# Optimization experiments

Measured on AMD Instinct MI355X. Metric: run time of the kernel, lower is better.

Reference implementation:

```python
import jax, jax.numpy as jnp
import numpy as np

B, N, C, K, TOPK = 16, 4096, 256, 8, 2
EPS = 1e-6
RATIO = 0.1      # gate_geno_ratio
TEMP = 1.0       # gate_temperature


def setup_inputs() -> dict:
    key = jax.random.key(0)
    ks = jax.random.split(key, 8)
    s = np.float32(1.0 / np.sqrt(C))  # ~xavier scale for C->C linears
    return {
        "tokens": jax.random.normal(ks[0], (B, N, C), jnp.float32),
        "geno_vec": jax.random.normal(ks[1], (B, C), jnp.float32),
        # gate params (gate_proj init std=0.001; gate_geno given small random instead of exact-zero init so it contributes)
        "Wg": jax.random.normal(ks[2], (K, C), jnp.float32) * 0.001,
        "bg": jnp.zeros((K,), jnp.float32),
        "Wgg": jax.random.normal(ks[3], (K, C), jnp.float32) * 0.001,
        "bgg": jnp.zeros((K,), jnp.float32),
        # per-expert 2-layer MLP params (dropout inactive in eval)
        "W1": jax.random.normal(ks[4], (K, C, C), jnp.float32) * s,
        "b1": jnp.zeros((K, C), jnp.float32),
        "W2": jax.random.normal(ks[5], (K, C, C), jnp.float32) * s,
        "b2": jnp.zeros((K, C), jnp.float32),
    }


def reference(tokens, geno_vec, Wg, bg, Wgg, bgg, W1, b1, W2, b2):
    # gate logits: [B,N,K]
    logits = jnp.einsum("bnc,kc->bnk", tokens, Wg) + bg
    logits = logits + RATIO * (geno_vec @ Wgg.T + bgg)[:, None, :]
    logits = logits / TEMP

    topv, topi = jax.lax.top_k(logits, TOPK)          # [B,N,TOPK]
    topw = jax.nn.softmax(topv, axis=-1)
    topw = jnp.maximum(topw, EPS)
    topw = topw / topw.sum(-1, keepdims=True)

    # dense gate weight matrix W: [B,N,K] (scatter of topw at topi; topk indices are distinct)
    hot = jax.nn.one_hot(topi, K, dtype=tokens.dtype)  # [B,N,TOPK,K]
    Wmat = (hot * topw[..., None]).sum(-2)             # [B,N,K]

    # load-balance loss on hard usage (detached in original)
    usage = jax.lax.stop_gradient(hot.sum(-2).mean((0, 1)))  # [K]
    lb_loss = (jnp.std(usage) / (usage.mean() + EPS)) ** 2

    mass_sum = Wmat.sum(axis=1)                        # [B,K]

    # per-expert MLP computed densely over all tokens; zero gate weight kills
    # non-routed tokens exactly (same math as gather->MLP->scatter-add)
    def expert_center(k):
        h = jax.nn.relu(tokens @ W1[k].T + b1[k])      # [B,N,C]
        out = h @ W2[k].T + b2[k]                      # [B,N,C]
        return jnp.einsum("bn,bnc->bc", Wmat[:, :, k], out)

    centers_sum = jnp.stack([expert_center(k) for k in range(K)], axis=1)  # [B,K,C]
    centers = centers_sum / jnp.maximum(mass_sum, EPS)[..., None]

    routing_confidence = (topv[:, :, 0] - topv[:, :, 1]).mean()
    return centers, lb_loss, routing_confidence
```

## Files before the change

### kernel.cpp

```cpp
#include <hip/hip_runtime.h>

#define B_ 16
#define N_ 4096
#define C_ 256
#define K_ 8
#define EPS 1e-6f
#define RATIO 0.1f

typedef float f32x4 __attribute__((ext_vector_type(4)));
typedef __bf16 bf16x8 __attribute__((ext_vector_type(8)));

__device__ inline unsigned short f2bf(float f){
  unsigned int u = __float_as_uint(f);
  u += 0x7FFFu + ((u >> 16) & 1u);
  return (unsigned short)(u >> 16);
}
__device__ inline float bf2f(unsigned short h){
  return __uint_as_float(((unsigned int)h) << 16);
}

union BFu { ushort4 u4[2]; bf16x8 v; };

__global__ __launch_bounds__(256) void k0_prep(
    const float* __restrict__ W1, const float* __restrict__ Wg,
    const float* __restrict__ geno, const float* __restrict__ Wgg,
    const float* __restrict__ bgg,
    unsigned short* __restrict__ W1swz,
    unsigned short* __restrict__ Wgp_hi, unsigned short* __restrict__ Wgp_lo,
    int* __restrict__ cnt,
    float* __restrict__ mass, float* __restrict__ conf,
    float* __restrict__ glog)
{
  int gid = blockIdx.x * 256 + threadIdx.x;
  if (gid < B_*K_) { cnt[gid] = 0; mass[gid] = 0.f; }
  if (gid == 0) conf[0] = 0.f;
  {
    int o = gid << 3;
    int lane6 = (o >> 3) & 63;
    int s  = (o >> 9) & 7;
    int nt = (o >> 12) & 15;
    int k  = o >> 16;
    int quad = lane6 >> 4, l16 = lane6 & 15;
    int j  = nt*16 + l16;
    int c0 = s*32 + quad*8;
    const float* src = W1 + (k << 16) + (j << 8) + c0;
    unsigned short* dst = W1swz + o;
    #pragma unroll
    for (int e = 0; e < 8; ++e) dst[e] = f2bf(src[e]);
  }
  if (gid < 16*C_){
    int r = gid >> 8, c = gid & 255;
    float v = (r < K_) ? Wg[(r << 8) + c] : 0.f;
    unsigned short h = f2bf(v);
    Wgp_hi[gid] = h;
    Wgp_lo[gid] = f2bf(v - bf2f(h));
  }
  int wv = gid >> 6;
  if (wv < B_*K_){
    int lane = threadIdx.x & 63;
    int b = wv >> 3, k = wv & 7;
    float4 a = *(const float4*)(geno + b*C_ + lane*4);
    float4 w = *(const float4*)(Wgg  + k*C_ + lane*4);
    float p = a.x*w.x + a.y*w.y + a.z*w.z + a.w*w.w;
    #pragma unroll
    for (int off = 32; off; off >>= 1) p += __shfl_xor(p, off);
    if (lane == 0) glog[wv] = RATIO * (p + bgg[k]);
  }
}

__global__ __launch_bounds__(256) void k1_gate(
    const float* __restrict__ tokens,
    const unsigned short* __restrict__ Wgp_hi, const unsigned short* __restrict__ Wgp_lo,
    const float* __restrict__ bg, const float* __restrict__ glog,
    int* __restrict__ cnt, int* __restrict__ bidx, float* __restrict__ bw,
    float* __restrict__ mass, float* __restrict__ conf,
    unsigned short* __restrict__ tok_bf)
{
  __shared__ float ls[64][9];
  __shared__ float bg_s[K_], gl_s[K_], mass_s[K_];
  __shared__ int lcnt[K_], gbase[K_];
  __shared__ int e0s[64], e1s[64], s0s[64], s1s[64];
  __shared__ float w0s[64], w1s[64];
  __shared__ float cred[4];
  int tid = threadIdx.x, lane = tid & 63, wave = tid >> 6;
  int quad = lane >> 4, l16 = lane & 15;
  int b = blockIdx.x >> 6;
  int tok0 = (blockIdx.x & 63) * 64;
  if (tid < K_){ bg_s[tid] = bg[tid]; gl_s[tid] = glog[b*K_ + tid];
                 mass_s[tid] = 0.f; lcnt[tid] = 0; }
  __syncthreads();

  {
    int trow = tok0 + wave*16 + l16;
    const float* xsrc = tokens + ((size_t)b*N_ + trow)*C_ + quad*8;
    unsigned short* bdst = tok_bf + (((size_t)(b*N_ + trow)) << 8) + quad*8;
    f32x4 xa[8], xb[8];
    #pragma unroll
    for (int s = 0; s < 8; ++s){
      xa[s] = *(const f32x4*)(xsrc + s*32);
      xb[s] = *(const f32x4*)(xsrc + s*32 + 4);
    }
    asm volatile("" : "+v"(xa[0]), "+v"(xa[1]), "+v"(xa[2]), "+v"(xa[3]),
                      "+v"(xa[4]), "+v"(xa[5]), "+v"(xa[6]), "+v"(xa[7]));
    asm volatile("" : "+v"(xb[0]), "+v"(xb[1]), "+v"(xb[2]), "+v"(xb[3]),
                      "+v"(xb[4]), "+v"(xb[5]), "+v"(xb[6]), "+v"(xb[7]));
    f32x4 acc; acc.x = 0.f; acc.y = 0.f; acc.z = 0.f; acc.w = 0.f;
    #pragma unroll
    for (int s = 0; s < 8; ++s){
      BFu hi, lo;
      hi.u4[0].x = f2bf(xa[s][0]); hi.u4[0].y = f2bf(xa[s][1]);
      hi.u4[0].z = f2bf(xa[s][2]); hi.u4[0].w = f2bf(xa[s][3]);
      hi.u4[1].x = f2bf(xb[s][0]); hi.u4[1].y = f2bf(xb[s][1]);
      hi.u4[1].z = f2bf(xb[s][2]); hi.u4[1].w = f2bf(xb[s][3]);
      lo.u4[0].x = f2bf(xa[s][0] - bf2f(hi.u4[0].x));
      lo.u4[0].y = f2bf(xa[s][1] - bf2f(hi.u4[0].y));
      lo.u4[0].z = f2bf(xa[s][2] - bf2f(hi.u4[0].z));
      lo.u4[0].w = f2bf(xa[s][3] - bf2f(hi.u4[0].w));
      lo.u4[1].x = f2bf(xb[s][0] - bf2f(hi.u4[1].x));
      lo.u4[1].y = f2bf(xb[s][1] - bf2f(hi.u4[1].y));
      lo.u4[1].z = f2bf(xb[s][2] - bf2f(hi.u4[1].z));
      lo.u4[1].w = f2bf(xb[s][3] - bf2f(hi.u4[1].w));
      *(ushort4*)(bdst + s*32)     = hi.u4[0];
      *(ushort4*)(bdst + s*32 + 4) = hi.u4[1];
      bf16x8 bhi = *(const bf16x8*)(Wgp_hi + l16*C_ + s*32 + quad*8);
      bf16x8 blo = *(const bf16x8*)(Wgp_lo + l16*C_ + s*32 + quad*8);
      acc = __builtin_amdgcn_mfma_f32_16x16x32_bf16(hi.v, bhi, acc, 0, 0, 0);
      acc = __builtin_amdgcn_mfma_f32_16x16x32_bf16(lo.v, bhi, acc, 0, 0, 0);
      acc = __builtin_amdgcn_mfma_f32_16x16x32_bf16(hi.v, blo, acc, 0, 0, 0);
    }
    if (l16 < K_){
      #pragma unroll
      for (int rr = 0; rr < 4; ++rr){
        int tl = wave*16 + quad*4 + rr;
        ls[tl][l16] = acc[rr] + bg_s[l16] + gl_s[l16];
      }
    }
  }
  __syncthreads();

  if (quad == 0){
    int t = (wave << 4) | l16;
    float v0 = -1e30f, v1 = -1e30f; int i0 = 0, i1 = 0;
    #pragma unroll
    for (int kk = 0; kk < K_; ++kk){
      float l = ls[t][kk];
      if (l > v0){ v1 = v0; i1 = i0; v0 = l; i0 = kk; }
      else if (l > v1){ v1 = l; i1 = kk; }
    }
    float e  = expf(v1 - v0);
    float w0 = 1.f / (1.f + e), w1 = e / (1.f + e);
    w0 = fmaxf(w0, EPS); w1 = fmaxf(w1, EPS);
    float inv = 1.f / (w0 + w1);
    w0 *= inv; w1 *= inv;
    int p0 = atomicAdd(&lcnt[i0], 1);
    int p1 = atomicAdd(&lcnt[i1], 1);
    e0s[t] = i0; e1s[t] = i1; s0s[t] = p0; s1s[t] = p1;
    w0s[t] = w0; w1s[t] = w1;
    atomicAdd(&mass_s[i0], w0);
    atomicAdd(&mass_s[i1], w1);
    float ca = v0 - v1;
    #pragma unroll
    for (int off = 8; off; off >>= 1) ca += __shfl_down(ca, off);
    if (l16 == 0) cred[wave] = ca;
  }
  __syncthreads();
  if (tid < K_){
    gbase[tid] = atomicAdd(&cnt[b*K_ + tid], lcnt[tid]);
    atomicAdd(&mass[b*K_ + tid], mass_s[tid]);
  }
  if (tid == 0) atomicAdd(conf, cred[0] + cred[1] + cred[2] + cred[3]);
  __syncthreads();
  if (quad == 0){
    int t = (wave << 4) | l16;
    int n = tok0 + t;
    int ke0 = e0s[t], ke1 = e1s[t];
    size_t o0 = (size_t)(b*K_ + ke0)*N_ + gbase[ke0] + s0s[t];
    size_t o1 = (size_t)(b*K_ + ke1)*N_ + gbase[ke1] + s1s[t];
    bidx[o0] = n;  bw[o0] = w0s[t];
    bidx[o1] = n;  bw[o1] = w1s[t];
  }
}

#define K4_STAGE(T, REG) do {                                                  \
    _Pragma("unroll")                                                          \
    for (int i = 0; i < 2; ++i){                                               \
      int c16 = (T)*512 + i*256 + tid;                                         \
      __builtin_amdgcn_global_load_lds(                                        \
        (const __attribute__((address_space(1))) unsigned int*)(wsrc + c16*8), \
        (__attribute__((address_space(3))) unsigned int*)(&Bs[REG][0] + (i*256 + tid)*8), \
        16, 0, 0);                                                             \
    }                                                                          \
  } while(0)

__global__ __launch_bounds__(256, 4) void k4_expert(
    const unsigned short* __restrict__ tok_bf, const unsigned short* __restrict__ W1swz,
    const float* __restrict__ b1, const int* __restrict__ cnt,
    const int* __restrict__ bidx, const float* __restrict__ bw,
    float* __restrict__ gpart)
{
  __shared__ unsigned short Bs[4][4096];
  __shared__ float wtok[128];
  __shared__ float red[2][4][16];
  __shared__ int Pb[129];

  int tid = threadIdx.x, lane = tid & 63, wave = tid >> 6;
  int quad = lane >> 4, l16 = lane & 15;

  if (wave == 0){
    int b2i = lane << 1;
    int cA = (cnt[b2i] + 127) >> 7;
    int cB = (cnt[b2i + 1] + 127) >> 7;
    int s = cA + cB;
    int ps = s;
    #pragma unroll
    for (int off = 1; off < 64; off <<= 1){
      int t = __shfl_up(ps, off);
      if (lane >= off) ps += t;
    }
    Pb[b2i]     = ps - s;
    Pb[b2i + 1] = ps - cB;
    if (lane == 63) Pb[128] = ps;
  }
  __syncthreads();

  int T = Pb[128];
  int lin = blockIdx.x;
  int wq = (lin & 7) * 144 + (lin >> 3);
  if (wq >= T) return;
  int lo = 0, hi = 128;
  #pragma unroll
  for (int it = 0; it < 7; ++it){
    int mid = (lo + hi) >> 1;
    if (Pb[mid] <= wq) lo = mid; else hi = mid;
  }
  int bucket = lo;
  int chunk = wq - Pb[lo];
  int bat = bucket >> 3, k = bucket & 7;
  int M = cnt[bucket];
  int Mm1 = M - 1;
  int bwbase = bucket << 12;

  const unsigned short* wsrc = W1swz + ((size_t)k << 16);

  K4_STAGE(0, 0);
  K4_STAGE(1, 1);

  if (tid < 128){
    int tn = chunk*128 + tid;
    wtok[tid] = (tn < M) ? bw[bwbase + tn] : 0.f;
  }

  int r0 = chunk*128 + (wave << 4) + l16;
  int nn0 = bidx[bwbase + min(r0, Mm1)];
  int nn1 = bidx[bwbase + min(r0 + 64, Mm1)];
  const unsigned short* p0 = tok_bf + (((size_t)((bat << 12) + nn0)) << 8) + (quad << 3);
  const unsigned short* p1 = tok_bf + (((size_t)((bat << 12) + nn1)) << 8) + (quad << 3);
  bf16x8 a0[8], a1[8];
  #pragma unroll
  for (int s = 0; s < 8; ++s){
    a0[s] = *(const bf16x8*)(p0 + s*32);
    a1[s] = *(const bf16x8*)(p1 + s*32);
  }

  float bias[16];
  #pragma unroll
  for (int p = 0; p < 16; ++p) bias[p] = b1[(k << 8) + (p << 4) + l16];

  float* gdst = gpart + (size_t)(((bucket << 5) + chunk) << 8);
  int wq4 = (wave << 4) + (quad << 2);

  #pragma unroll
  for (int p = 0; p < 16; ++p){
    if (p < 14){
      K4_STAGE(p + 2, (p + 2) & 3);
      asm volatile("s_waitcnt vmcnt(4) lgkmcnt(0)" ::: "memory");
    } else if (p == 14){
      asm volatile("s_waitcnt vmcnt(2) lgkmcnt(0)" ::: "memory");
    } else {
      asm volatile("s_waitcnt vmcnt(0) lgkmcnt(0)" ::: "memory");
    }
    __builtin_amdgcn_s_barrier();

    if (p > 0 && tid < 16){
      int pb = (p - 1) & 1;
      float sv = red[pb][0][tid] + red[pb][1][tid]
               + red[pb][2][tid] + red[pb][3][tid];
      gdst[((p - 1) << 4) + tid] = sv;
    }

    f32x4 acc0, acc1;
    acc0.x=0.f; acc0.y=0.f; acc0.z=0.f; acc0.w=0.f;
    acc1.x=0.f; acc1.y=0.f; acc1.z=0.f; acc1.w=0.f;
    #pragma unroll
    for (int s = 0; s < 8; ++s){
      bf16x8 bb = *(const bf16x8*)(&Bs[p & 3][0] + ((s*64 + lane) << 3));
      acc0 = __builtin_amdgcn_mfma_f32_16x16x32_bf16(a0[s], bb, acc0, 0, 0, 0);
      acc1 = __builtin_amdgcn_mfma_f32_16x16x32_bf16(a1[s], bb, acc1, 0, 0, 0);
    }
    float pt = 0.f;
    #pragma unroll
    for (int rr = 0; rr < 4; ++rr){
      float h0 = fmaxf(acc0[rr] + bias[p], 0.f);
      float h1 = fmaxf(acc1[rr] + bias[p], 0.f);
      pt += wtok[wq4 + rr] * h0 + wtok[64 + wq4 + rr] * h1;
    }
    pt += __shfl_down(pt, 32);
    pt += __shfl_down(pt, 16);
    if (lane < 16) red[p & 1][wave][lane] = pt;
  }
  asm volatile("s_waitcnt lgkmcnt(0)" ::: "memory");
  __builtin_amdgcn_s_barrier();
  if (tid < 16){
    float sv = red[1][0][tid] + red[1][1][tid] + red[1][2][tid] + red[1][3][tid];
    gdst[(15 << 4) + tid] = sv;
  }
}

__global__ __launch_bounds__(256) void k5_centers(
    const float* __restrict__ gpart, const int* __restrict__ cnt,
    const float* __restrict__ W2, const float* __restrict__ b2,
    const float* __restrict__ mass, const float* __restrict__ conf,
    float* __restrict__ out)
{
  __shared__ float gv[C_];
  int z = blockIdx.x, tid = threadIdx.x;
  int k = z & 7;
  int nch = (cnt[z] + 127) >> 7;
  float sv = 0.f;
  for (int c = 0; c < nch; ++c)
    sv += gpart[(size_t)((((z << 5) + c) << 8) + tid)];
  gv[tid] = sv;
  __syncthreads();
  float m = mass[z];
  float inv = 1.f / fmaxf(m, EPS);
  int tq = tid & 3, cb = tid >> 2;
  #pragma unroll 1
  for (int h = 0; h < 2; ++h){
    int c = (blockIdx.y*2 + h)*64 + cb;
    const float4* wrow = (const float4*)(W2 + ((((k << 8) + c)) << 8));
    float dot = 0.f;
    #pragma unroll
    for (int jj = 0; jj < 16; ++jj){
      float4 w4 = wrow[jj*4 + tq];
      float4 g4 = *(const float4*)&gv[(jj*4 + tq) * 4];
      dot += w4.x*g4.x + w4.y*g4.y + w4.z*g4.z + w4.w*g4.w;
    }
    dot += __shfl_xor(dot, 1);
    dot += __shfl_xor(dot, 2);
    if (tq == 0) out[z*C_ + c] = (dot + m * b2[k*C_ + c]) * inv;
  }
  if (z == 0 && blockIdx.y == 0 && tid == 0){
    float u[K_];
    #pragma unroll
    for (int kk = 0; kk < K_; ++kk) u[kk] = 0.f;
    for (int i = 0; i < B_*K_; ++i) u[i & 7] += (float)cnt[i];
    float mean = 0.f;
    #pragma unroll
    for (int kk = 0; kk < K_; ++kk){ u[kk] *= (1.f / (float)(B_*N_)); mean += u[kk]; }
    mean *= (1.f / K_);
    float var = 0.f;
    #pragma unroll
    for (int kk = 0; kk < K_; ++kk){ float d = u[kk] - mean; var += d*d; }
    var *= (1.f / K_);
    float denom = mean + EPS;
    out[B_*K_*C_]     = var / (denom * denom);
    out[B_*K_*C_ + 1] = conf[0] / (float)(B_*N_);
  }
}

extern "C" void kernel_launch(void* const* d_in, const int* in_sizes, int n_in,
                              void* d_out, int out_size, void* d_ws, size_t ws_size,
                              hipStream_t stream)
{
  const float* tokens = (const float*)d_in[0];
  const float* geno   = (const float*)d_in[1];
  const float* Wg     = (const float*)d_in[2];
  const float* bg     = (const float*)d_in[3];
  const float* Wgg    = (const float*)d_in[4];
  const float* bgg    = (const float*)d_in[5];
  const float* W1     = (const float*)d_in[6];
  const float* b1     = (const float*)d_in[7];
  const float* W2     = (const float*)d_in[8];
  const float* b2     = (const float*)d_in[9];
  float* out = (float*)d_out;
  char* ws = (char*)d_ws;
  unsigned short* W1swz  = (unsigned short*)(ws);
  unsigned short* Wgp_hi = (unsigned short*)(ws + 1048576);
  unsigned short* Wgp_lo = (unsigned short*)(ws + 1056768);
  float* glog = (float*)(ws + 1196032);
  int*   cnt  = (int*)  (ws + 1196544);
  float* mass = (float*)(ws + 1197056);
  float* conf = (float*)(ws + 1197568);
  int*   bidx = (int*)  (ws + 1198080);
  float* bw   = (float*)(ws + 3295232);
  unsigned short* tok_bf = (unsigned short*)(ws + 5392384);
  float* gpart = (float*)(ws + 38946816);

  k0_prep<<<256, 256, 0, stream>>>(W1, Wg, geno, Wgg, bgg, W1swz, Wgp_hi, Wgp_lo,
                                   cnt, mass, conf, glog);
  k1_gate<<<1024, 256, 0, stream>>>(tokens, Wgp_hi, Wgp_lo, bg, glog,
                                    cnt, bidx, bw, mass, conf, tok_bf);
  k4_expert<<<1152, 256, 0, stream>>>(tok_bf, W1swz, b1, cnt, bidx, bw, gpart);
  k5_centers<<<dim3(128, 2), 256, 0, stream>>>(gpart, cnt, W2, b2, mass, conf, out);
}
```

Measured before the change: 178.7 us.

## Fuse prep into gate kernel and replace global atomics with deterministic prefix pass

The prep kernel is merged into the gate kernel: each block converts its slice of W1, builds the hi/lo bf16 split of Wg in shared memory, and computes the geno logits itself. Global atomic counters are replaced by per-block counts plus a small prefix-sum kernel that scatters packed (index, weight) pairs into the expert buckets. The expert kernel reads these packed pairs, drops from four to three LDS stage buffers, and raises its occupancy hint. This trades the cross-block atomics and one launch for an extra tokexp round trip and a 16-block serial scatter kernel with limited parallelism.

```diff
diff --git a/kernel.cpp b/kernel.cpp
--- a/kernel.cpp
+++ b/kernel.cpp
@@ -21,73 +21,66 @@
 
 union BFu { ushort4 u4[2]; bf16x8 v; };
 
-__global__ __launch_bounds__(256) void k0_prep(
-    const float* __restrict__ W1, const float* __restrict__ Wg,
-    const float* __restrict__ geno, const float* __restrict__ Wgg,
-    const float* __restrict__ bgg,
-    unsigned short* __restrict__ W1swz,
-    unsigned short* __restrict__ Wgp_hi, unsigned short* __restrict__ Wgp_lo,
-    int* __restrict__ cnt,
-    float* __restrict__ mass, float* __restrict__ conf,
-    float* __restrict__ glog)
+__global__ __launch_bounds__(256) void kA_gate(
+    const float* __restrict__ tokens, const float* __restrict__ geno,
+    const float* __restrict__ Wg, const float* __restrict__ bg,
+    const float* __restrict__ Wgg, const float* __restrict__ bgg,
+    const float* __restrict__ W1,
+    unsigned short* __restrict__ W1swz, unsigned short* __restrict__ tok_bf,
+    uint2* __restrict__ tokexp, int* __restrict__ lcnt_blk,
+    float* __restrict__ mass_blk, float* __restrict__ conf_blk)
 {
-  int gid = blockIdx.x * 256 + threadIdx.x;
-  if (gid < B_*K_) { cnt[gid] = 0; mass[gid] = 0.f; }
-  if (gid == 0) conf[0] = 0.f;
-  {
-    int o = gid << 3;
+  __shared__ float ls[64][9];
+  __shared__ unsigned short wgh[4096], wgl[4096];
+  __shared__ float bg_s[K_], gl_s[K_], mass_s[K_];
+  __shared__ int lcnt[K_];
+  __shared__ float cred[4];
+  int tid = threadIdx.x, lane = tid & 63, wave = tid >> 6;
+  int quad = lane >> 4, l16 = lane & 15;
+  int blk = blockIdx.x;
+  int b = blk >> 6;
+  int tok0 = (blk & 63) * 64;
+
+  if (tid < 64){
+    int g = blk*64 + tid;
+    int o = g << 3;
     int lane6 = (o >> 3) & 63;
     int s  = (o >> 9) & 7;
     int nt = (o >> 12) & 15;
     int k  = o >> 16;
-    int quad = lane6 >> 4, l16 = lane6 & 15;
-    int j  = nt*16 + l16;
-    int c0 = s*32 + quad*8;
-    const float* src = W1 + (k << 16) + (j << 8) + c0;
+    int q2 = lane6 >> 4, r16 = lane6 & 15;
+    const float* src = W1 + (k << 16) + ((nt*16 + r16) << 8) + s*32 + q2*8;
     unsigned short* dst = W1swz + o;
     #pragma unroll
     for (int e = 0; e < 8; ++e) dst[e] = f2bf(src[e]);
   }
-  if (gid < 16*C_){
-    int r = gid >> 8, c = gid & 255;
-    float v = (r < K_) ? Wg[(r << 8) + c] : 0.f;
-    unsigned short h = f2bf(v);
-    Wgp_hi[gid] = h;
-    Wgp_lo[gid] = f2bf(v - bf2f(h));
-  }
-  int wv = gid >> 6;
-  if (wv < B_*K_){
-    int lane = threadIdx.x & 63;
-    int b = wv >> 3, k = wv & 7;
-    float4 a = *(const float4*)(geno + b*C_ + lane*4);
-    float4 w = *(const float4*)(Wgg  + k*C_ + lane*4);
-    float p = a.x*w.x + a.y*w.y + a.z*w.z + a.w*w.w;
-    #pragma unroll
-    for (int off = 32; off; off >>= 1) p += __shfl_xor(p, off);
-    if (lane == 0) glog[wv] = RATIO * (p + bgg[k]);
-  }
-}
-
-__global__ __launch_bounds__(256) void k1_gate(
-    const float* __restrict__ tokens,
-    const unsigned short* __restrict__ Wgp_hi, const unsigned short* __restrict__ Wgp_lo,
-    const float* __restrict__ bg, const float* __restrict__ glog,
-    int* __restrict__ cnt, int* __restrict__ bidx, float* __restrict__ bw,
-    float* __restrict__ mass, float* __restrict__ conf,
-    unsigned short* __restrict__ tok_bf)
-{
-  __shared__ float ls[64][9];
-  __shared__ float bg_s[K_], gl_s[K_], mass_s[K_];
-  __shared__ int lcnt[K_], gbase[K_];
-  __shared__ int e0s[64], e1s[64], s0s[64], s1s[64];
-  __shared__ float w0s[64], w1s[64];
-  __shared__ float cred[4];
-  int tid = threadIdx.x, lane = tid & 63, wave = tid >> 6;
-  int quad = lane >> 4, l16 = lane & 15;
-  int b = blockIdx.x >> 6;
-  int tok0 = (blockIdx.x & 63) * 64;
-  if (tid < K_){ bg_s[tid] = bg[tid]; gl_s[tid] = glog[b*K_ + tid];
-                 mass_s[tid] = 0.f; lcnt[tid] = 0; }
+  {
+    f32x4 wa = *(const f32x4*)(Wg + tid*8);
+    f32x4 wb = *(const f32x4*)(Wg + tid*8 + 4);
+    #pragma unroll
+    for (int e = 0; e < 4; ++e){
+      unsigned short h = f2bf(wa[e]);
+      wgh[tid*8 + e] = h;  wgl[tid*8 + e] = f2bf(wa[e] - bf2f(h));
+      unsigned short h2 = f2bf(wb[e]);
+      wgh[tid*8 + 4 + e] = h2;  wgl[tid*8 + 4 + e] = f2bf(wb[e] - bf2f(h2));
+      wgh[2048 + tid*8 + e] = 0;      wgl[2048 + tid*8 + e] = 0;
+      wgh[2048 + tid*8 + 4 + e] = 0;  wgl[2048 + tid*8 + 4 + e] = 0;
+    }
+  }
+  if (tid < K_){ bg_s[tid] = bg[tid]; mass_s[tid] = 0.f; lcnt[tid] = 0; }
+  {
+    int k = wave*2 + (lane >> 5);
+    int hl = lane & 31;
+    f32x4 a0 = *(const f32x4*)(geno + b*C_ + hl*8);
+    f32x4 a1 = *(const f32x4*)(geno + b*C_ + hl*8 + 4);
+    f32x4 w0v = *(const f32x4*)(Wgg + k*C_ + hl*8);
+    f32x4 w1v = *(const f32x4*)(Wgg + k*C_ + hl*8 + 4);
+    float p = a0[0]*w0v[0] + a0[1]*w0v[1] + a0[2]*w0v[2] + a0[3]*w0v[3]
+            + a1[0]*w1v[0] + a1[1]*w1v[1] + a1[2]*w1v[2] + a1[3]*w1v[3];
+    #pragma unroll
+    for (int off = 16; off; off >>= 1) p += __shfl_xor(p, off);
+    if (hl == 0) gl_s[k] = RATIO * (p + bgg[k]);
+  }
   __syncthreads();
 
   {
@@ -122,8 +115,8 @@
       lo.u4[1].w = f2bf(xb[s][3] - bf2f(hi.u4[1].w));
       *(ushort4*)(bdst + s*32)     = hi.u4[0];
       *(ushort4*)(bdst + s*32 + 4) = hi.u4[1];
-      bf16x8 bhi = *(const bf16x8*)(Wgp_hi + l16*C_ + s*32 + quad*8);
-      bf16x8 blo = *(const bf16x8*)(Wgp_lo + l16*C_ + s*32 + quad*8);
+      bf16x8 bhi = *(const bf16x8*)(wgh + l16*C_ + s*32 + quad*8);
+      bf16x8 blo = *(const bf16x8*)(wgl + l16*C_ + s*32 + quad*8);
       acc = __builtin_amdgcn_mfma_f32_16x16x32_bf16(hi.v, bhi, acc, 0, 0, 0);
       acc = __builtin_amdgcn_mfma_f32_16x16x32_bf16(lo.v, bhi, acc, 0, 0, 0);
       acc = __builtin_amdgcn_mfma_f32_16x16x32_bf16(hi.v, blo, acc, 0, 0, 0);
@@ -154,10 +147,11 @@
     w0 *= inv; w1 *= inv;
     int p0 = atomicAdd(&lcnt[i0], 1);
     int p1 = atomicAdd(&lcnt[i1], 1);
-    e0s[t] = i0; e1s[t] = i1; s0s[t] = p0; s1s[t] = p1;
-    w0s[t] = w0; w1s[t] = w1;
     atomicAdd(&mass_s[i0], w0);
     atomicAdd(&mass_s[i1], w1);
+    tokexp[(size_t)b*N_ + tok0 + t] =
+      make_uint2((unsigned)(i0 | (i1 << 4) | (p0 << 8) | (p1 << 16)),
+                 __float_as_uint(w0));
     float ca = v0 - v1;
     #pragma unroll
     for (int off = 8; off; off >>= 1) ca += __shfl_down(ca, off);
@@ -165,19 +159,57 @@
   }
   __syncthreads();
   if (tid < K_){
-    gbase[tid] = atomicAdd(&cnt[b*K_ + tid], lcnt[tid]);
-    atomicAdd(&mass[b*K_ + tid], mass_s[tid]);
-  }
-  if (tid == 0) atomicAdd(conf, cred[0] + cred[1] + cred[2] + cred[3]);
-  __syncthreads();
-  if (quad == 0){
-    int t = (wave << 4) | l16;
-    int n = tok0 + t;
-    int ke0 = e0s[t], ke1 = e1s[t];
-    size_t o0 = (size_t)(b*K_ + ke0)*N_ + gbase[ke0] + s0s[t];
-    size_t o1 = (size_t)(b*K_ + ke1)*N_ + gbase[ke1] + s1s[t];
-    bidx[o0] = n;  bw[o0] = w0s[t];
-    bidx[o1] = n;  bw[o1] = w1s[t];
+    lcnt_blk[blk*K_ + tid] = lcnt[tid];
+    mass_blk[blk*K_ + tid] = mass_s[tid];
+  }
+  if (tid == 0) conf_blk[blk] = cred[0] + cred[1] + cred[2] + cred[3];
+}
+
+__global__ __launch_bounds__(256) void kP_prefix(
+    const int* __restrict__ lcnt_blk, const float* __restrict__ mass_blk,
+    const float* __restrict__ conf_blk, const uint2* __restrict__ tokexp,
+    int* __restrict__ cnt, float* __restrict__ mass,
+    float* __restrict__ conf_b, uint2* __restrict__ bwi)
+{
+  __shared__ int bp[64][K_];
+  __shared__ int tot[K_];
+  int b = blockIdx.x, tid = threadIdx.x, lane = tid & 63, wave = tid >> 6;
+  if (wave == 0){
+    #pragma unroll
+    for (int k = 0; k < K_; ++k){
+      int v = lcnt_blk[(b*64 + lane)*K_ + k];
+      int ps = v;
+      #pragma unroll
+      for (int off = 1; off < 64; off <<= 1){
+        int t = __shfl_up(ps, off);
+        if (lane >= off) ps += t;
+      }
+      bp[lane][k] = ps - v;
+      if (lane == 63) tot[k] = ps;
+      float mv = mass_blk[(b*64 + lane)*K_ + k];
+      #pragma unroll
+      for (int off = 32; off; off >>= 1) mv += __shfl_xor(mv, off);
+      if (lane == 0) mass[b*K_ + k] = mv;
+    }
+    float cv = conf_blk[b*64 + lane];
+    #pragma unroll
+    for (int off = 32; off; off >>= 1) cv += __shfl_xor(cv, off);
+    if (lane == 0) conf_b[b] = cv;
+  }
+  __syncthreads();
+  if (tid < K_) cnt[b*K_ + tid] = tot[tid];
+  #pragma unroll 1
+  for (int it = 0; it < 16; ++it){
+    int n = it*256 + tid;
+    uint2 te = tokexp[(size_t)b*N_ + n];
+    int e0 = te.x & 15, e1 = (te.x >> 4) & 15;
+    int p0 = (te.x >> 8) & 255, p1 = (te.x >> 16) & 255;
+    int j = n >> 6;
+    float w0 = __uint_as_float(te.y);
+    float w1 = 1.f - w0;
+    bwi[(size_t)(b*K_ + e0)*N_ + bp[j][e0] + p0] = make_uint2((unsigned)n, te.y);
+    bwi[(size_t)(b*K_ + e1)*N_ + bp[j][e1] + p1] =
+      make_uint2((unsigned)n, __float_as_uint(w1));
   }
 }
 
@@ -192,13 +224,12 @@
     }                                                                          \
   } while(0)
 
-__global__ __launch_bounds__(256, 4) void k4_expert(
+__global__ __launch_bounds__(256, 5) void k4_expert(
     const unsigned short* __restrict__ tok_bf, const unsigned short* __restrict__ W1swz,
     const float* __restrict__ b1, const int* __restrict__ cnt,
-    const int* __restrict__ bidx, const float* __restrict__ bw,
-    float* __restrict__ gpart)
+    const uint2* __restrict__ bwi, float* __restrict__ gpart)
 {
-  __shared__ unsigned short Bs[4][4096];
+  __shared__ unsigned short Bs[3][4096];
   __shared__ float wtok[128];
   __shared__ float red[2][4][16];
   __shared__ int Pb[129];
@@ -238,7 +269,7 @@
   int bat = bucket >> 3, k = bucket & 7;
   int M = cnt[bucket];
   int Mm1 = M - 1;
-  int bwbase = bucket << 12;
+  size_t bwbase = (size_t)bucket * N_;
 
   const unsigned short* wsrc = W1swz + ((size_t)k << 16);
 
@@ -247,12 +278,14 @@
 
   if (tid < 128){
     int tn = chunk*128 + tid;
-    wtok[tid] = (tn < M) ? bw[bwbase + tn] : 0.f;
+    uint2 e = bwi[bwbase + min(tn, Mm1)];
+    wtok[tid] = (tn < M) ? __uint_as_float(e.y) : 0.f;
   }
 
   int r0 = chunk*128 + (wave << 4) + l16;
-  int nn0 = bidx[bwbase + min(r0, Mm1)];
-  int nn1 = bidx[bwbase + min(r0 + 64, Mm1)];
+  uint2 ev0 = bwi[bwbase + min(r0, Mm1)];
+  uint2 ev1 = bwi[bwbase + min(r0 + 64, Mm1)];
+  int nn0 = (int)ev0.x, nn1 = (int)ev1.x;
   const unsigned short* p0 = tok_bf + (((size_t)((bat << 12) + nn0)) << 8) + (quad << 3);
   const unsigned short* p1 = tok_bf + (((size_t)((bat << 12) + nn1)) << 8) + (quad << 3);
   bf16x8 a0[8], a1[8];
@@ -271,14 +304,8 @@
 
   #pragma unroll
   for (int p = 0; p < 16; ++p){
-    if (p < 14){
-      K4_STAGE(p + 2, (p + 2) & 3);
-      asm volatile("s_waitcnt vmcnt(4) lgkmcnt(0)" ::: "memory");
-    } else if (p == 14){
-      asm volatile("s_waitcnt vmcnt(2) lgkmcnt(0)" ::: "memory");
-    } else {
-      asm volatile("s_waitcnt vmcnt(0) lgkmcnt(0)" ::: "memory");
-    }
+    if (p < 15) asm volatile("s_waitcnt vmcnt(2) lgkmcnt(0)" ::: "memory");
+    else        asm volatile("s_waitcnt vmcnt(0) lgkmcnt(0)" ::: "memory");
     __builtin_amdgcn_s_barrier();
 
     if (p > 0 && tid < 16){
@@ -287,13 +314,14 @@
                + red[pb][2][tid] + red[pb][3][tid];
       gdst[((p - 1) << 4) + tid] = sv;
     }
+    if (p <= 13) K4_STAGE(p + 2, (p + 2) % 3);
 
     f32x4 acc0, acc1;
     acc0.x=0.f; acc0.y=0.f; acc0.z=0.f; acc0.w=0.f;
     acc1.x=0.f; acc1.y=0.f; acc1.z=0.f; acc1.w=0.f;
     #pragma unroll
     for (int s = 0; s < 8; ++s){
-      bf16x8 bb = *(const bf16x8*)(&Bs[p & 3][0] + ((s*64 + lane) << 3));
+      bf16x8 bb = *(const bf16x8*)(&Bs[p % 3][0] + ((s*64 + lane) << 3));
       acc0 = __builtin_amdgcn_mfma_f32_16x16x32_bf16(a0[s], bb, acc0, 0, 0, 0);
       acc1 = __builtin_amdgcn_mfma_f32_16x16x32_bf16(a1[s], bb, acc1, 0, 0, 0);
     }
@@ -319,7 +347,7 @@
 __global__ __launch_bounds__(256) void k5_centers(
     const float* __restrict__ gpart, const int* __restrict__ cnt,
     const float* __restrict__ W2, const float* __restrict__ b2,
-    const float* __restrict__ mass, const float* __restrict__ conf,
+    const float* __restrict__ mass, const float* __restrict__ conf_b,
     float* __restrict__ out)
 {
   __shared__ float gv[C_];
@@ -363,8 +391,10 @@
     for (int kk = 0; kk < K_; ++kk){ float d = u[kk] - mean; var += d*d; }
     var *= (1.f / K_);
     float denom = mean + EPS;
+    float cs = 0.f;
+    for (int i = 0; i < B_; ++i) cs += conf_b[i];
     out[B_*K_*C_]     = var / (denom * denom);
-    out[B_*K_*C_ + 1] = conf[0] / (float)(B_*N_);
+    out[B_*K_*C_ + 1] = cs / (float)(B_*N_);
   }
 }
 
@@ -384,22 +414,24 @@
   const float* b2     = (const float*)d_in[9];
   float* out = (float*)d_out;
   char* ws = (char*)d_ws;
-  unsigned short* W1swz  = (unsigned short*)(ws);
-  unsigned short* Wgp_hi = (unsigned short*)(ws + 1048576);
-  unsigned short* Wgp_lo = (unsigned short*)(ws + 1056768);
-  float* glog = (float*)(ws + 1196032);
-  int*   cnt  = (int*)  (ws + 1196544);
-  float* mass = (float*)(ws + 1197056);
-  float* conf = (float*)(ws + 1197568);
-  int*   bidx = (int*)  (ws + 1198080);
-  float* bw   = (float*)(ws + 3295232);
-  unsigned short* tok_bf = (unsigned short*)(ws + 5392384);
-  float* gpart = (float*)(ws + 38946816);
-
-  k0_prep<<<256, 256, 0, stream>>>(W1, Wg, geno, Wgg, bgg, W1swz, Wgp_hi, Wgp_lo,
-                                   cnt, mass, conf, glog);
-  k1_gate<<<1024, 256, 0, stream>>>(tokens, Wgp_hi, Wgp_lo, bg, glog,
-                                    cnt, bidx, bw, mass, conf, tok_bf);
-  k4_expert<<<1152, 256, 0, stream>>>(tok_bf, W1swz, b1, cnt, bidx, bw, gpart);
-  k5_centers<<<dim3(128, 2), 256, 0, stream>>>(gpart, cnt, W2, b2, mass, conf, out);
-}
+  unsigned short* W1swz = (unsigned short*)(ws);
+  uint2* tokexp   = (uint2*)(ws + 1048576);
+  int*   lcnt_blk = (int*)  (ws + 1572864);
+  float* mass_blk = (float*)(ws + 1605632);
+  float* conf_blk = (float*)(ws + 1638400);
+  float* conf_b   = (float*)(ws + 1642496);
+  int*   cnt      = (int*)  (ws + 1642560);
+  float* mass     = (float*)(ws + 1643072);
+  uint2* bwi      = (uint2*)(ws + 1643584);
+  unsigned short* tok_bf = (unsigned short*)(ws + 5837888);
+  float* gpart    = (float*)(ws + 39392320);
+
+  kA_gate<<<1024, 256, 0, stream>>>(tokens, geno, Wg, bg, Wgg, bgg, W1,
+                                    W1swz, tok_bf, tokexp, lcnt_blk,
+                                    mass_blk, conf_blk);
+  kP_prefix<<<16, 256, 0, stream>>>(lcnt_blk, mass_blk, conf_blk, tokexp,
+                                    cnt, mass, conf_b, bwi);
+  k4_expert<<<1152, 256, 0, stream>>>(tok_bf, W1swz, b1, cnt, bwi, gpart);
+  k5_centers<<<dim3(128, 2), 256, 0, stream>>>(gpart, cnt, W2, b2, mass,
+                                               conf_b, out);
+}
```

Measured after the change: 212.0 us. 18.6% more time.
